# Kernel optimization log

Hardware: AMD Instinct MI355X
Metric: run time of the kernel (lower is better)

## Reference

```python
import jax, jax.numpy as jnp
import numpy as np

D = 512; NH = 8; NL = 6; DFF = 2048
TOK = 1024; APP = 3; V = TOK + APP; PAD = V - 1
B = 256; SENC = 16; LTGT = 62


def setup_inputs() -> dict:
    key = jax.random.key(0)
    ks = jax.random.split(key, 14)
    g = lambda k, shp, s=0.02: jax.random.normal(k, shp, jnp.float32) * s
    return dict(
        encoder_out=jax.random.normal(ks[0], (B, SENC, D), jnp.float32),
        point_out=jax.random.normal(ks[1], (B, D), jnp.float32),
        emb=g(ks[2], (V, D)),
        pos_embed=g(ks[3], (1, LTGT, D)),
        sa_inw=g(ks[4], (NL, 3 * D, D)), sa_inb=jnp.zeros((NL, 3 * D), jnp.float32),
        sa_outw=g(ks[5], (NL, D, D)), sa_outb=jnp.zeros((NL, D), jnp.float32),
        ca_inw=g(ks[6], (NL, 3 * D, D)), ca_inb=jnp.zeros((NL, 3 * D), jnp.float32),
        ca_outw=g(ks[7], (NL, D, D)), ca_outb=jnp.zeros((NL, D), jnp.float32),
        ln1_s=jnp.ones((NL, D), jnp.float32), ln1_b=jnp.zeros((NL, D), jnp.float32),
        ln2_s=jnp.ones((NL, D), jnp.float32), ln2_b=jnp.zeros((NL, D), jnp.float32),
        ln3_s=jnp.ones((NL, D), jnp.float32), ln3_b=jnp.zeros((NL, D), jnp.float32),
        ff1_w=g(ks[8], (NL, DFF, D)), ff1_b=jnp.zeros((NL, DFF), jnp.float32),
        ff2_w=g(ks[9], (NL, D, DFF)), ff2_b=jnp.zeros((NL, D), jnp.float32),
        out_w=g(ks[10], (V, D)), out_b=jnp.zeros((V,), jnp.float32),
        tgt=jax.random.randint(ks[11], (B, LTGT), 0, TOK),
    )


def _ln(x, s, b, eps=1e-5):
    m = x.mean(-1, keepdims=True)
    v = ((x - m) ** 2).mean(-1, keepdims=True)
    return (x - m) / jnp.sqrt(v + eps) * s + b


def _mha(q_in, kv_in, inw, inb, outw, outb, mask):
    # PyTorch MultiheadAttention with packed in_proj [3D, D]
    hd = D // NH
    wq, wk, wv = inw[:D], inw[D:2 * D], inw[2 * D:]
    bq, bk, bv = inb[:D], inb[D:2 * D], inb[2 * D:]
    Bq, Tq = q_in.shape[0], q_in.shape[1]
    Tk = kv_in.shape[1]
    q = (q_in @ wq.T + bq).reshape(Bq, Tq, NH, hd)
    k = (kv_in @ wk.T + bk).reshape(Bq, Tk, NH, hd)
    v = (kv_in @ wv.T + bv).reshape(Bq, Tk, NH, hd)
    s = jnp.einsum('bqhd,bkhd->bhqk', q, k) / np.float32(np.sqrt(hd))
    if mask is not None:
        s = s + mask
    a = jax.nn.softmax(s, axis=-1)
    o = jnp.einsum('bhqk,bkhd->bqhd', a, v).reshape(Bq, Tq, D)
    return o @ outw.T + outb


def reference(encoder_out, point_out, emb, pos_embed,
              sa_inw, sa_inb, sa_outw, sa_outb,
              ca_inw, ca_inb, ca_outw, ca_outb,
              ln1_s, ln1_b, ln2_s, ln2_b, ln3_s, ln3_b,
              ff1_w, ff1_b, ff2_w, ff2_b, out_w, out_b, tgt):
    # scheduled_sampling_ratio == 1.0 => the per-step loop always writes the
    # ground-truth token, so output_sequence == tgt[:, :-1] and the returned
    # tensor equals one full causal decoder pass over tgt[:, :-1].
    tokens = tgt[:, :-1]                      # [B, L], L = 61
    L = tokens.shape[1]
    neg = jnp.float32(-jnp.inf)
    causal = jnp.where(jnp.triu(jnp.ones((L, L), bool), 1), neg, 0.0)
    padm = jnp.where(tokens == PAD, neg, 0.0)[:, None, None, :]  # [B,1,1,L]
    mask = causal[None, None] + padm          # [B,1,L,L]
    mem = encoder_out[:, :1, :]               # memory length 1 (encoder_out[:, [0]])
    x = emb[tokens] + point_out[:, None, :] + pos_embed[0, :L]
    for i in range(NL):
        x = _ln(x + _mha(x, x, sa_inw[i], sa_inb[i], sa_outw[i], sa_outb[i], mask), ln1_s[i], ln1_b[i])
        x = _ln(x + _mha(x, mem, ca_inw[i], ca_inb[i], ca_outw[i], ca_outb[i], None), ln2_s[i], ln2_b[i])
        h = jax.nn.relu(x @ ff1_w[i].T + ff1_b[i]) @ ff2_w[i].T + ff2_b[i]
        x = _ln(x + h, ln3_s[i], ln3_b[i])
    return x @ out_w.T + out_b               # [B, L, V]
```

## Files before the change

kernel.cpp:

```cpp
#include <hip/hip_runtime.h>
#include <stdint.h>
#include <stddef.h>

typedef unsigned short u16;
typedef float f4 __attribute__((ext_vector_type(4)));
typedef float f32x4 __attribute__((ext_vector_type(4)));
typedef short bf16x8 __attribute__((ext_vector_type(8)));
typedef u16 u16x4 __attribute__((ext_vector_type(4)));
typedef int i4v __attribute__((ext_vector_type(4)));

#define PAD_TOK 1026
#define LQ 61
#define NBATCH 256
#define MTOT (NBATCH * LQ)

__device__ __forceinline__ u16 f2b(float f) {
  uint32_t x = __float_as_uint(f);
  x += 0x7fff + ((x >> 16) & 1);
  return (u16)(x >> 16);
}
__device__ __forceinline__ float b2f(u16 u) {
  return __uint_as_float(((uint32_t)u) << 16);
}
__device__ __forceinline__ u16x4 cvt4(f4 v) {
  return (u16x4){f2b(v[0]), f2b(v[1]), f2b(v[2]), f2b(v[3])};
}

#define GLDS(gptr, lptr) __builtin_amdgcn_global_load_lds( \
    (const __attribute__((address_space(1))) void*)(gptr), \
    (__attribute__((address_space(3))) void*)(lptr), 16, 0, 0)

__device__ __forceinline__ bf16x8 ldfrag(const u16* buf, int row, int ksl, int kg) {
  const int chunk = (ksl * 4 + kg) ^ (row & 7);
  return *(const bf16x8*)&buf[row * 64 + chunk * 8];
}

__global__ __launch_bounds__(512) void gemm_bt2(
    const u16* __restrict__ A, const u16* __restrict__ W,
    const float* __restrict__ bias,
    float* __restrict__ Cf, u16* __restrict__ Cb,
    int N, int K, int Nreal, int ldc, int relu)
{
  __shared__ u16 SH[384 * 64];
  u16* const As = SH;
  u16* const Bs = SH + 8192;

  const int gx = gridDim.x;
  const int nwg = gx * gridDim.y;
  const int orig = blockIdx.y * gx + blockIdx.x;
  const int q8 = nwg >> 3, r8 = nwg & 7;
  const int xcd = orig & 7, off = orig >> 3;
  const int nid = (xcd < r8 ? xcd * (q8 + 1) : r8 * (q8 + 1) + (xcd - r8) * q8) + off;
  const int bx = nid % gx, by = nid / gx;

  const int tid = threadIdx.x;
  const int wid = tid >> 6, lane = tid & 63;
  const int wm = wid >> 2, wn = wid & 3;
  const long m0 = (long)by * 128;
  const long n0 = (long)bx * 256;

  const int lr = lane >> 3;
  const int lc = lane & 7;
  const int scol = ((lc ^ lr) << 3);

  f32x4 acc[4][4];
#pragma unroll
  for (int i = 0; i < 4; ++i)
#pragma unroll
    for (int j = 0; j < 4; ++j) acc[i][j] = (f32x4){0.f, 0.f, 0.f, 0.f};

  const u16* Abase = A + m0 * K;
  const u16* Wbase = W + n0 * K;
  const int r = lane & 15, kg = lane >> 4;

  for (int kt = 0; kt < K; kt += 64) {
#pragma unroll
    for (int c = 0; c < 2; ++c) {
      const int row = wid * 16 + c * 8;
      GLDS(Abase + (long)(row + lr) * K + kt + scol, &As[row * 64]);
    }
#pragma unroll
    for (int c = 0; c < 4; ++c) {
      const int row = wid * 32 + c * 8;
      GLDS(Wbase + (long)(row + lr) * K + kt + scol, &Bs[row * 64]);
    }
    __syncthreads();

#pragma unroll
    for (int ks = 0; ks < 2; ++ks) {
      bf16x8 a[4], b[4];
#pragma unroll
      for (int mi = 0; mi < 4; ++mi)
        a[mi] = ldfrag(As, wm * 64 + mi * 16 + r, ks, kg);
#pragma unroll
      for (int ni = 0; ni < 4; ++ni)
        b[ni] = ldfrag(Bs, wn * 64 + ni * 16 + r, ks, kg);
#pragma unroll
      for (int mi = 0; mi < 4; ++mi)
#pragma unroll
        for (int ni = 0; ni < 4; ++ni)
          acc[mi][ni] = __builtin_amdgcn_mfma_f32_16x16x32_bf16(a[mi], b[ni], acc[mi][ni], 0, 0, 0);
    }
    __syncthreads();
  }

  const int cr4 = (lane >> 4) * 4;
  const int cc = lane & 15;

  if (Cb) {
#pragma unroll
    for (int half = 0; half < 2; ++half) {
      if (wm == half) {
#pragma unroll
        for (int ni = 0; ni < 4; ++ni) {
          const int coll = wn * 64 + ni * 16 + cc;
          const float bv = bias[(int)n0 + coll];
#pragma unroll
          for (int mi = 0; mi < 4; ++mi) {
#pragma unroll
            for (int j = 0; j < 4; ++j) {
              const int rowl = mi * 16 + cr4 + j;
              float v = acc[mi][ni][j] + bv;
              if (relu) v = fmaxf(v, 0.f);
              const int phys = (coll >> 3) ^ (rowl & 31);
              SH[rowl * 256 + phys * 8 + (coll & 7)] = f2b(v);
            }
          }
        }
      }
      __syncthreads();
#pragma unroll
      for (int i = 0; i < 4; ++i) {
        const int t = i * 512 + tid;
        const int row = t >> 5, ch = t & 31;
        const int n = (int)n0 + ch * 8;
        if (n < Nreal) {
          const int phys = ch ^ (row & 31);
          *(bf16x8*)&Cb[(m0 + half * 64 + row) * (long)N + n] =
              *(const bf16x8*)&SH[row * 256 + phys * 8];
        }
      }
      __syncthreads();
    }
  } else {
    float* SHf = (float*)SH;
#pragma unroll
    for (int q = 0; q < 4; ++q) {
      if (wm == (q >> 1)) {
        const int mib = (q & 1) * 2;
#pragma unroll
        for (int ni = 0; ni < 4; ++ni) {
          const int coll = wn * 64 + ni * 16 + cc;
          const float bv = bias[(int)n0 + coll];
#pragma unroll
          for (int mi2 = 0; mi2 < 2; ++mi2) {
#pragma unroll
            for (int j = 0; j < 4; ++j) {
              const int rowl = mi2 * 16 + cr4 + j;
              float v = acc[mib + mi2][ni][j] + bv;
              if (relu) v = fmaxf(v, 0.f);
              SHf[rowl * 260 + coll] = v;
            }
          }
        }
      }
      __syncthreads();
      {
        const int row = tid >> 4, c = tid & 15;
        const int nbase = (int)n0 + c * 16;
        const long gro = (m0 + q * 32 + row) * (long)ldc;
        if (nbase + 16 <= Nreal) {
#pragma unroll
          for (int e = 0; e < 16; ++e)
            Cf[gro + nbase + e] = SHf[row * 260 + c * 16 + e];
        } else if (nbase < Nreal) {
          for (int e = 0; e < Nreal - nbase; ++e)
            Cf[gro + nbase + e] = SHf[row * 260 + c * 16 + e];
        }
      }
      __syncthreads();
    }
  }
}

__global__ __launch_bounds__(512) void gemm_bt3(
    const u16* __restrict__ A, const u16* __restrict__ W,
    const float* __restrict__ bias, u16* __restrict__ Cb,
    int N, int K, int relu)
{
  __shared__ u16 SH[320 * 64];
  u16* const As = SH;
  u16* const Bs = SH + 4096;

  const int gx = gridDim.x;
  const int nwg = gx * gridDim.y;
  const int orig = blockIdx.y * gx + blockIdx.x;
  const int q8 = nwg >> 3, r8 = nwg & 7;
  const int xcd = orig & 7, off = orig >> 3;
  const int nid = (xcd < r8 ? xcd * (q8 + 1) : r8 * (q8 + 1) + (xcd - r8) * q8) + off;
  const int bx = nid % gx, by = nid / gx;

  const int tid = threadIdx.x;
  const int wid = tid >> 6, lane = tid & 63;
  const int wm = wid >> 2, wn = wid & 3;
  const long m0 = (long)by * 64;
  const long n0 = (long)bx * 256;

  const int lr = lane >> 3;
  const int lc = lane & 7;
  const int scol = ((lc ^ lr) << 3);

  f32x4 acc[2][4];
#pragma unroll
  for (int i = 0; i < 2; ++i)
#pragma unroll
    for (int j = 0; j < 4; ++j) acc[i][j] = (f32x4){0.f, 0.f, 0.f, 0.f};

  const u16* Abase = A + m0 * K;
  const u16* Wbase = W + n0 * K;
  const int r = lane & 15, kg = lane >> 4;

  for (int kt = 0; kt < K; kt += 64) {
    {
      const int arow = wid * 8;
      GLDS(Abase + (long)(arow + lr) * K + kt + scol, &As[arow * 64]);
#pragma unroll
      for (int c = 0; c < 4; ++c) {
        const int row = wid * 32 + c * 8;
        GLDS(Wbase + (long)(row + lr) * K + kt + scol, &Bs[row * 64]);
      }
    }
    __syncthreads();

#pragma unroll
    for (int ks = 0; ks < 2; ++ks) {
      bf16x8 a0 = ldfrag(As, wm * 32 + r, ks, kg);
      bf16x8 a1 = ldfrag(As, wm * 32 + 16 + r, ks, kg);
#pragma unroll
      for (int ni = 0; ni < 4; ++ni) {
        bf16x8 b = ldfrag(Bs, wn * 64 + ni * 16 + r, ks, kg);
        acc[0][ni] = __builtin_amdgcn_mfma_f32_16x16x32_bf16(a0, b, acc[0][ni], 0, 0, 0);
        acc[1][ni] = __builtin_amdgcn_mfma_f32_16x16x32_bf16(a1, b, acc[1][ni], 0, 0, 0);
      }
    }
    __syncthreads();
  }

  const int cr4 = (lane >> 4) * 4;
  const int cc = lane & 15;

#pragma unroll
  for (int ni = 0; ni < 4; ++ni) {
    const int coll = wn * 64 + ni * 16 + cc;
    const float bv = bias[(int)n0 + coll];
#pragma unroll
    for (int mi = 0; mi < 2; ++mi) {
#pragma unroll
      for (int j = 0; j < 4; ++j) {
        const int rowl = wm * 32 + mi * 16 + cr4 + j;
        float v = acc[mi][ni][j] + bv;
        if (relu) v = fmaxf(v, 0.f);
        const int phys = (coll >> 3) ^ (rowl & 31);
        SH[rowl * 256 + phys * 8 + (coll & 7)] = f2b(v);
      }
    }
  }
  __syncthreads();
#pragma unroll
  for (int i = 0; i < 4; ++i) {
    const int t = i * 512 + tid;
    const int row = t >> 5, ch = t & 31;
    const int n = (int)n0 + ch * 8;
    const int phys = ch ^ (row & 31);
    *(bf16x8*)&Cb[(m0 + row) * (long)N + n] =
        *(const bf16x8*)&SH[row * 256 + phys * 8];
  }
}

template<int BM>
__global__ __launch_bounds__(256) void gemm_bt(
    const u16* __restrict__ A, const u16* __restrict__ W,
    const float* __restrict__ bias,
    float* __restrict__ Cf, u16* __restrict__ Cb,
    int M, int N, int K, int Nreal, int ldc, int relu,
    long aZ, long wZ, long bZ, long cZ)
{
  constexpr int MI = BM / 32;
  const int z = blockIdx.z;
  A += z * aZ; W += z * wZ; bias += z * bZ;
  if (Cf) Cf += z * cZ;
  if (Cb) Cb += z * cZ;

  __shared__ u16 As[BM * 64];
  __shared__ u16 Bs[128 * 64];

  const int gx = gridDim.x;
  const int nwg = gx * gridDim.y;
  const int orig = blockIdx.y * gx + blockIdx.x;
  const int q8 = nwg >> 3, r8 = nwg & 7;
  const int xcd = orig & 7, off = orig >> 3;
  const int nid = (xcd < r8 ? xcd * (q8 + 1) : r8 * (q8 + 1) + (xcd - r8) * q8) + off;
  const int bx = nid % gx, by = nid / gx;

  const int tid = threadIdx.x;
  const int wid = tid >> 6, lane = tid & 63;
  const int wr = wid >> 1, wc = wid & 1;
  const long m0 = (long)by * BM;
  const long n0 = (long)bx * 128;

  const int lr = lane >> 3;
  const int lc = lane & 7;
  const int scol = ((lc ^ lr) << 3);

  f32x4 acc[MI][4];
#pragma unroll
  for (int i = 0; i < MI; ++i)
#pragma unroll
    for (int j = 0; j < 4; ++j) acc[i][j] = (f32x4){0.f, 0.f, 0.f, 0.f};

  const u16* Abase = A + m0 * K;
  const u16* Wbase = W + n0 * K;
  const int r = lane & 15, kg = lane >> 4;

  for (int kt = 0; kt < K; kt += 64) {
#pragma unroll
    for (int c = 0; c < BM / 32; ++c) {
      const int row = wid * (BM / 4) + c * 8;
      GLDS(Abase + (long)(row + lr) * K + kt + scol, &As[row * 64]);
    }
#pragma unroll
    for (int c = 0; c < 4; ++c) {
      const int row = wid * 32 + c * 8;
      GLDS(Wbase + (long)(row + lr) * K + kt + scol, &Bs[row * 64]);
    }
    __syncthreads();

#pragma unroll
    for (int ks = 0; ks < 2; ++ks) {
      bf16x8 a[MI], b[4];
#pragma unroll
      for (int mi = 0; mi < MI; ++mi)
        a[mi] = ldfrag(As, wr * (BM / 2) + mi * 16 + r, ks, kg);
#pragma unroll
      for (int ni = 0; ni < 4; ++ni)
        b[ni] = ldfrag(Bs, wc * 64 + ni * 16 + r, ks, kg);
#pragma unroll
      for (int mi = 0; mi < MI; ++mi)
#pragma unroll
        for (int ni = 0; ni < 4; ++ni)
          acc[mi][ni] = __builtin_amdgcn_mfma_f32_16x16x32_bf16(a[mi], b[ni], acc[mi][ni], 0, 0, 0);
    }
    __syncthreads();
  }

  const int cr4 = (lane >> 4) * 4;
  const int cc = lane & 15;

  if (Cb) {
#pragma unroll
    for (int ni = 0; ni < 4; ++ni) {
      const int coll = wc * 64 + ni * 16 + cc;
      const float bv = bias[(int)n0 + coll];
#pragma unroll
      for (int mi = 0; mi < MI; ++mi) {
#pragma unroll
        for (int j = 0; j < 4; ++j) {
          const int rowl = wr * (BM / 2) + mi * 16 + cr4 + j;
          float v = acc[mi][ni][j] + bv;
          if (relu) v = fmaxf(v, 0.f);
          const int sw = (rowl & 7) << 3;
          u16* half = (coll & 64) ? Bs : As;
          half[rowl * 64 + ((coll & 63) ^ sw)] = f2b(v);
        }
      }
    }
    __syncthreads();
    constexpr int PT = BM / 16;
#pragma unroll
    for (int i = 0; i < PT; ++i) {
      const int t = i * 256 + tid;
      const int row = t >> 4, ch = t & 15;
      const int n = (int)n0 + ch * 8;
      if (n < Nreal) {
        const int phys = (ch & 7) ^ (row & 7);
        const u16* half = (ch < 8) ? As : Bs;
        bf16x8 vv = *(const bf16x8*)&half[row * 64 + phys * 8];
        *(bf16x8*)&Cb[(m0 + row) * (long)N + n] = vv;
      }
    }
  } else {
#pragma unroll
    for (int ni = 0; ni < 4; ++ni) {
      const int n = (int)n0 + wc * 64 + ni * 16 + cc;
      if (n >= Nreal) continue;
      const float bv = bias[n];
#pragma unroll
      for (int mi = 0; mi < MI; ++mi) {
#pragma unroll
        for (int j = 0; j < 4; ++j) {
          const long m = m0 + wr * (BM / 2) + mi * 16 + cr4 + j;
          float v = acc[mi][ni][j] + bv;
          if (relu) v = fmaxf(v, 0.f);
          Cf[m * ldc + n] = v;
        }
      }
    }
  }
}

__global__ __launch_bounds__(512) void gemmln_k(
    const u16* __restrict__ A, const u16* __restrict__ W,
    const float* __restrict__ bias,
    const u16* __restrict__ cavb,
    const float* __restrict__ s1w, const float* __restrict__ b1w,
    const float* __restrict__ s2w, const float* __restrict__ b2w,
    u16* __restrict__ XB, int K)
{
  __shared__ u16 LDSBUF[2][36864];
  __shared__ float LSTAT[64][8];
  __shared__ u16 LCAV[1536];
  u16* const EP = &LDSBUF[0][0];

  const int nwg = gridDim.x;
  const int orig = blockIdx.x;
  const int q8 = nwg >> 3, r8 = nwg & 7;
  const int xcd = orig & 7, off = orig >> 3;
  const int by = (xcd < r8 ? xcd * (q8 + 1) : r8 * (q8 + 1) + (xcd - r8) * q8) + off;

  const int tid = threadIdx.x;
  const int wid = tid >> 6, lane = tid & 63;
  const int wm = wid >> 2, wn = wid & 3;
  const long m0 = (long)by * 64;

  const int lr = lane >> 3, lc = lane & 7;
  const int scol = ((lc ^ lr) << 3);
  const int r = lane & 15, kg = lane >> 4;

  f32x4 acc[2][8];
#pragma unroll
  for (int i = 0; i < 2; ++i)
#pragma unroll
    for (int j = 0; j < 8; ++j) acc[i][j] = (f32x4){0.f, 0.f, 0.f, 0.f};

  const u16* Abase = A + m0 * K;

#define STAGE(buf, kt) do {                                              \
    const int arow_ = wid * 8;                                           \
    GLDS(Abase + (long)(arow_ + lr) * K + (kt) + scol,                   \
         &(buf)[32768 + arow_ * 64]);                                    \
    _Pragma("unroll")                                                    \
    for (int c_ = 0; c_ < 8; ++c_) {                                     \
      const int row_ = wid * 64 + c_ * 8;                                \
      GLDS(W + (long)(row_ + lr) * K + (kt) + scol, &(buf)[row_ * 64]);  \
    }                                                                    \
  } while (0)

  const int nt = K >> 6;
  STAGE(LDSBUF[0], 0);
  asm volatile("s_waitcnt vmcnt(0)" ::: "memory");
  __builtin_amdgcn_sched_barrier(0);
  __builtin_amdgcn_s_barrier();

  for (int t = 0; t < nt; ++t) {
    u16* const bufc = &LDSBUF[t & 1][0];
    if (t + 1 < nt) STAGE(LDSBUF[(t + 1) & 1], (t + 1) << 6);
#pragma unroll
    for (int ks = 0; ks < 2; ++ks) {
      bf16x8 a0 = ldfrag(bufc + 32768, wm * 32 + r, ks, kg);
      bf16x8 a1 = ldfrag(bufc + 32768, wm * 32 + 16 + r, ks, kg);
      __builtin_amdgcn_s_setprio(1);
#pragma unroll
      for (int ni = 0; ni < 8; ++ni) {
        bf16x8 b = ldfrag(bufc, wn * 128 + ni * 16 + r, ks, kg);
        acc[0][ni] = __builtin_amdgcn_mfma_f32_16x16x32_bf16(a0, b, acc[0][ni], 0, 0, 0);
        acc[1][ni] = __builtin_amdgcn_mfma_f32_16x16x32_bf16(a1, b, acc[1][ni], 0, 0, 0);
      }
      __builtin_amdgcn_s_setprio(0);
    }
    asm volatile("s_waitcnt vmcnt(0)" ::: "memory");
    __builtin_amdgcn_sched_barrier(0);
    __builtin_amdgcn_s_barrier();
  }
#undef STAGE

  const int b0 = (int)(m0 / LQ);
  const int bsplit1 = (b0 + 1) * LQ;
  const int bsplit2 = (b0 + 2) * LQ;

#pragma unroll
  for (int i = 0; i < 8; ++i) {
    const int t = i * 512 + tid;
    const int row = t >> 6, ch = t & 63;
    *(bf16x8*)&EP[row * 516 + ch * 8] =
        *(const bf16x8*)&XB[(m0 + row) * 512 + ch * 8];
  }
  for (int t = tid; t < 1536; t += 512) {
    const int bb = t >> 9, c = t & 511;
    int bi = b0 + bb;
    if (bi > NBATCH - 1) bi = NBATCH - 1;
    LCAV[bb * 512 + c] = cavb[(long)bi * 512 + c];
  }
  __syncthreads();

  float bcol[8];
#pragma unroll
  for (int ni = 0; ni < 8; ++ni) bcol[ni] = bias[wn * 128 + ni * 16 + r];
#pragma unroll
  for (int mi = 0; mi < 2; ++mi)
#pragma unroll
    for (int ni = 0; ni < 8; ++ni) {
      const int col = wn * 128 + ni * 16 + r;
#pragma unroll
      for (int j = 0; j < 4; ++j) {
        const int row = wm * 32 + mi * 16 + kg * 4 + j;
        acc[mi][ni][j] += bcol[ni] + b2f(EP[row * 516 + col]);
      }
    }

#pragma unroll
  for (int mi = 0; mi < 2; ++mi)
#pragma unroll
    for (int j = 0; j < 4; ++j) {
      float s1 = 0.f, s2 = 0.f;
#pragma unroll
      for (int ni = 0; ni < 8; ++ni) {
        const float v = acc[mi][ni][j];
        s1 += v; s2 += v * v;
      }
#pragma unroll
      for (int o = 1; o < 16; o <<= 1) {
        s1 += __shfl_xor(s1, o);
        s2 += __shfl_xor(s2, o);
      }
      if (r == 0) {
        const int row = wm * 32 + mi * 16 + kg * 4 + j;
        LSTAT[row][wn] = s1;
        LSTAT[row][4 + wn] = s2;
      }
    }
  __syncthreads();

  float sc[8], bc[8];
#pragma unroll
  for (int ni = 0; ni < 8; ++ni) {
    const int col = wn * 128 + ni * 16 + r;
    sc[ni] = s1w[col]; bc[ni] = b1w[col];
  }
#pragma unroll
  for (int mi = 0; mi < 2; ++mi)
#pragma unroll
    for (int j = 0; j < 4; ++j) {
      const int row = wm * 32 + mi * 16 + kg * 4 + j;
      const float S1 = LSTAT[row][0] + LSTAT[row][1] + LSTAT[row][2] + LSTAT[row][3];
      const float S2 = LSTAT[row][4] + LSTAT[row][5] + LSTAT[row][6] + LSTAT[row][7];
      const float mean = S1 * (1.f / 512.f);
      const float var = S2 * (1.f / 512.f) - mean * mean;
      const float rstd = rsqrtf(var + 1e-5f);
#pragma unroll
      for (int ni = 0; ni < 8; ++ni)
        acc[mi][ni][j] = (acc[mi][ni][j] - mean) * rstd * sc[ni] + bc[ni];
    }

#pragma unroll
  for (int mi = 0; mi < 2; ++mi)
#pragma unroll
    for (int j = 0; j < 4; ++j) {
      const int row = wm * 32 + mi * 16 + kg * 4 + j;
      const int gr = (int)m0 + row;
      const int sel = (gr >= bsplit2) ? 2 : ((gr >= bsplit1) ? 1 : 0);
#pragma unroll
      for (int ni = 0; ni < 8; ++ni) {
        const int col = wn * 128 + ni * 16 + r;
        acc[mi][ni][j] += b2f(LCAV[sel * 512 + col]);
      }
    }
  __syncthreads();
#pragma unroll
  for (int mi = 0; mi < 2; ++mi)
#pragma unroll
    for (int j = 0; j < 4; ++j) {
      float s1 = 0.f, s2 = 0.f;
#pragma unroll
      for (int ni = 0; ni < 8; ++ni) {
        const float v = acc[mi][ni][j];
        s1 += v; s2 += v * v;
      }
#pragma unroll
      for (int o = 1; o < 16; o <<= 1) {
        s1 += __shfl_xor(s1, o);
        s2 += __shfl_xor(s2, o);
      }
      if (r == 0) {
        const int row = wm * 32 + mi * 16 + kg * 4 + j;
        LSTAT[row][wn] = s1;
        LSTAT[row][4 + wn] = s2;
      }
    }
  __syncthreads();
#pragma unroll
  for (int ni = 0; ni < 8; ++ni) {
    const int col = wn * 128 + ni * 16 + r;
    sc[ni] = s2w[col]; bc[ni] = b2w[col];
  }
#pragma unroll
  for (int mi = 0; mi < 2; ++mi)
#pragma unroll
    for (int j = 0; j < 4; ++j) {
      const int row = wm * 32 + mi * 16 + kg * 4 + j;
      const float S1 = LSTAT[row][0] + LSTAT[row][1] + LSTAT[row][2] + LSTAT[row][3];
      const float S2 = LSTAT[row][4] + LSTAT[row][5] + LSTAT[row][6] + LSTAT[row][7];
      const float mean = S1 * (1.f / 512.f);
      const float var = S2 * (1.f / 512.f) - mean * mean;
      const float rstd = rsqrtf(var + 1e-5f);
#pragma unroll
      for (int ni = 0; ni < 8; ++ni)
        acc[mi][ni][j] = (acc[mi][ni][j] - mean) * rstd * sc[ni] + bc[ni];
    }

#pragma unroll
  for (int mi = 0; mi < 2; ++mi)
#pragma unroll
    for (int ni = 0; ni < 8; ++ni) {
      const int col = wn * 128 + ni * 16 + r;
#pragma unroll
      for (int j = 0; j < 4; ++j) {
        const int row = wm * 32 + mi * 16 + kg * 4 + j;
        EP[row * 516 + col] = f2b(acc[mi][ni][j]);
      }
    }
  __syncthreads();
#pragma unroll
  for (int i = 0; i < 8; ++i) {
    const int t = i * 512 + tid;
    const int row = t >> 6, ch = t & 63;
    *(bf16x8*)&XB[(m0 + row) * 512 + ch * 8] =
        *(const bf16x8*)&EP[row * 516 + ch * 8];
  }
}

__global__ __launch_bounds__(256) void attn_k(const u16* __restrict__ qkv,
                                              const int* __restrict__ tgt,
                                              u16* __restrict__ outp)
{
  __shared__ u16 Qs[64 * 72];
  __shared__ u16 Ks[64 * 72];
  __shared__ u16 Vt[64 * 72];
  __shared__ float S[64 * 65];
  __shared__ int stok[64];

  const int bid = blockIdx.x;
  const int b = bid >> 3, h = bid & 7;
  const int tid = threadIdx.x;
  const int tr = tid >> 2, seg = tid & 3;

  if (tid < 64) stok[tid] = (tid < 61) ? tgt[b * 62 + tid] : -1;

  const long rowbase = ((long)(b * LQ + tr)) * 1536 + h * 64;
  if (tr < LQ) {
    const i4v* qsrc = (const i4v*)(qkv + rowbase + seg * 16);
    i4v q0 = qsrc[0], q1 = qsrc[1];
    *(i4v*)&Qs[tr * 72 + seg * 16] = q0;
    *(i4v*)&Qs[tr * 72 + seg * 16 + 8] = q1;
    const i4v* ksrc = (const i4v*)(qkv + rowbase + 512 + seg * 16);
    i4v k0 = ksrc[0], k1 = ksrc[1];
    *(i4v*)&Ks[tr * 72 + seg * 16] = k0;
    *(i4v*)&Ks[tr * 72 + seg * 16 + 8] = k1;
    const u16* vsrc = qkv + rowbase + 1024 + seg * 16;
#pragma unroll
    for (int i = 0; i < 16; ++i) Vt[(seg * 16 + i) * 72 + tr] = vsrc[i];
  } else {
    i4v zz = {0, 0, 0, 0};
    *(i4v*)&Qs[tr * 72 + seg * 16] = zz;
    *(i4v*)&Qs[tr * 72 + seg * 16 + 8] = zz;
    *(i4v*)&Ks[tr * 72 + seg * 16] = zz;
    *(i4v*)&Ks[tr * 72 + seg * 16 + 8] = zz;
#pragma unroll
    for (int i = 0; i < 16; ++i) Vt[(seg * 16 + i) * 72 + tr] = 0;
  }
  __syncthreads();

  const int lane = tid & 63, w = tid >> 6;
  const int r = lane & 15, kg = lane >> 4;

  {
    f32x4 s[4];
#pragma unroll
    for (int ni = 0; ni < 4; ++ni) s[ni] = (f32x4){0.f, 0.f, 0.f, 0.f};
    bf16x8 a0 = *(const bf16x8*)&Qs[(w * 16 + r) * 72 + kg * 8];
    bf16x8 a1 = *(const bf16x8*)&Qs[(w * 16 + r) * 72 + 32 + kg * 8];
#pragma unroll
    for (int ni = 0; ni < 4; ++ni) {
      bf16x8 b0 = *(const bf16x8*)&Ks[(ni * 16 + r) * 72 + kg * 8];
      bf16x8 b1 = *(const bf16x8*)&Ks[(ni * 16 + r) * 72 + 32 + kg * 8];
      s[ni] = __builtin_amdgcn_mfma_f32_16x16x32_bf16(a0, b0, s[ni], 0, 0, 0);
      s[ni] = __builtin_amdgcn_mfma_f32_16x16x32_bf16(a1, b1, s[ni], 0, 0, 0);
    }
#pragma unroll
    for (int ni = 0; ni < 4; ++ni)
#pragma unroll
      for (int j = 0; j < 4; ++j)
        S[(w * 16 + kg * 4 + j) * 65 + ni * 16 + r] = s[ni][j];
  }
  __syncthreads();

  {
    const int row = tid >> 2, g = tid & 3;
    float vals[16];
    float mx = -3e38f;
#pragma unroll
    for (int i = 0; i < 16; ++i) {
      const int k = g * 16 + i;
      float v = S[row * 65 + k] * 0.125f;
      const bool ok = (k <= row) && (k < LQ) && (stok[k] != PAD_TOK);
      v = ok ? v : -1e30f;
      vals[i] = v;
      mx = fmaxf(mx, v);
    }
    mx = fmaxf(mx, __shfl_xor(mx, 1));
    mx = fmaxf(mx, __shfl_xor(mx, 2));
    float sum = 0.f;
#pragma unroll
    for (int i = 0; i < 16; ++i) { float e = __expf(vals[i] - mx); vals[i] = e; sum += e; }
    sum += __shfl_xor(sum, 1);
    sum += __shfl_xor(sum, 2);
    const float inv = 1.f / sum;
#pragma unroll
    for (int i = 0; i < 16; ++i) Qs[row * 72 + g * 16 + i] = f2b(vals[i] * inv);
  }
  __syncthreads();

  {
    f32x4 o[4];
#pragma unroll
    for (int ni = 0; ni < 4; ++ni) o[ni] = (f32x4){0.f, 0.f, 0.f, 0.f};
    bf16x8 a0 = *(const bf16x8*)&Qs[(w * 16 + r) * 72 + kg * 8];
    bf16x8 a1 = *(const bf16x8*)&Qs[(w * 16 + r) * 72 + 32 + kg * 8];
#pragma unroll
    for (int ni = 0; ni < 4; ++ni) {
      bf16x8 b0 = *(const bf16x8*)&Vt[(ni * 16 + r) * 72 + kg * 8];
      bf16x8 b1 = *(const bf16x8*)&Vt[(ni * 16 + r) * 72 + 32 + kg * 8];
      o[ni] = __builtin_amdgcn_mfma_f32_16x16x32_bf16(a0, b0, o[ni], 0, 0, 0);
      o[ni] = __builtin_amdgcn_mfma_f32_16x16x32_bf16(a1, b1, o[ni], 0, 0, 0);
    }
#pragma unroll
    for (int ni = 0; ni < 4; ++ni)
#pragma unroll
      for (int j = 0; j < 4; ++j) {
        const int qrow = w * 16 + kg * 4 + j;
        const int col = ni * 16 + r;
        Ks[qrow * 64 + (col ^ ((qrow & 7) << 3))] = f2b(o[ni][j]);
      }
  }
  __syncthreads();

  {
    const int row = tid >> 2, sub = tid & 3;
    if (row < LQ) {
      const long obase = ((long)(b * LQ + row)) * 512 + h * 64;
#pragma unroll
      for (int i = 0; i < 2; ++i) {
        const int ch = i * 4 + sub;
        const int phys = ch ^ (row & 7);
        bf16x8 vv = *(const bf16x8*)&Ks[row * 64 + phys * 8];
        *(bf16x8*)&outp[obase + ch * 8] = vv;
      }
    }
  }
}

__device__ __forceinline__ void ln_row(f4& v0, f4& v1,
                                       const float* __restrict__ sw,
                                       const float* __restrict__ bw, int d0) {
  float s1 = v0[0] + v0[1] + v0[2] + v0[3] + v1[0] + v1[1] + v1[2] + v1[3];
  float s2 = v0[0]*v0[0] + v0[1]*v0[1] + v0[2]*v0[2] + v0[3]*v0[3]
           + v1[0]*v1[0] + v1[1]*v1[1] + v1[2]*v1[2] + v1[3]*v1[3];
#pragma unroll
  for (int off = 1; off < 64; off <<= 1) {
    s1 += __shfl_xor(s1, off);
    s2 += __shfl_xor(s2, off);
  }
  const float mean = s1 * (1.f / 512.f);
  const float var = s2 * (1.f / 512.f) - mean * mean;
  const float rstd = rsqrtf(var + 1e-5f);
  const f4* sp = (const f4*)(sw + d0);
  const f4* bp = (const f4*)(bw + d0);
  f4 ss0 = sp[0], ss1 = sp[1], bb0 = bp[0], bb1 = bp[1];
#pragma unroll
  for (int i = 0; i < 4; ++i) {
    v0[i] = (v0[i] - mean) * rstd * ss0[i] + bb0[i];
    v1[i] = (v1[i] - mean) * rstd * ss1[i] + bb1[i];
  }
}

__global__ __launch_bounds__(256) void lnf3_k(const u16* __restrict__ p,
                                              const u16* __restrict__ xr,
                                              const float* __restrict__ s1,
                                              const float* __restrict__ b1,
                                              u16* __restrict__ out)
{
  const int m = blockIdx.x * 4 + (threadIdx.x >> 6);
  const int lane = threadIdx.x & 63;
  const int d0 = lane * 8;
  bf16x8 pv = *(const bf16x8*)(p + (long)m * 512 + d0);
  bf16x8 xv = *(const bf16x8*)(xr + (long)m * 512 + d0);
  f4 v0, v1;
#pragma unroll
  for (int i = 0; i < 4; ++i) {
    v0[i] = b2f((u16)pv[i]) + b2f((u16)xv[i]);
    v1[i] = b2f((u16)pv[4 + i]) + b2f((u16)xv[4 + i]);
  }
  ln_row(v0, v1, s1, b1, d0);
  u16x4* ob = (u16x4*)(out + (long)m * 512 + d0);
  ob[0] = cvt4(v0);
  ob[1] = cvt4(v1);
}

__global__ __launch_bounds__(256) void embed_k(const float* __restrict__ emb,
                                               const float* __restrict__ pout,
                                               const float* __restrict__ pos,
                                               const int* __restrict__ tgt,
                                               u16* __restrict__ XB)
{
  const int m = blockIdx.x * 4 + (threadIdx.x >> 6);
  const int lane = threadIdx.x & 63;
  const int b = m / LQ, t = m % LQ;
  const int tok = tgt[b * 62 + t];
  const int d0 = lane * 8;
  const f4* e = (const f4*)(emb + (long)tok * 512 + d0);
  const f4* p = (const f4*)(pout + (long)b * 512 + d0);
  const f4* q = (const f4*)(pos + (long)t * 512 + d0);
  f4 v0 = e[0] + p[0] + q[0];
  f4 v1 = e[1] + p[1] + q[1];
  u16x4* xb = (u16x4*)(XB + (long)m * 512 + d0);
  xb[0] = cvt4(v0);
  xb[1] = cvt4(v1);
}

__global__ void cvtall_k(const float* __restrict__ sa_inw, const float* __restrict__ sa_outw,
                         const float* __restrict__ ca_outw, const float* __restrict__ ff1_w,
                         const float* __restrict__ ff2_w, const float* __restrict__ ca_inw,
                         const float* __restrict__ out_w, const float* __restrict__ out_b,
                         const float* __restrict__ enc,
                         u16* __restrict__ WSA, u16* __restrict__ WSO,
                         u16* __restrict__ WCO, u16* __restrict__ WF1,
                         u16* __restrict__ WF2, u16* __restrict__ WCAV,
                         u16* __restrict__ WOUT, float* __restrict__ BOUT,
                         u16* __restrict__ MEMB)
{
  const int C0 = 320;
  const int C1 = C0 + 32768;
  const int C2 = C1 + 163840;
  const int C3 = C2 + 393216;
  const int C4 = C3 + 1179648;
  const int C5 = C4 + 393216;
  const int C6 = C5 + 393216;
  const int C7 = C6 + 1572864;
  const int C8 = C7 + 1572864;
  for (int i = blockIdx.x * 256 + threadIdx.x; i < C8; i += gridDim.x * 256) {
    if (i < C0) {
      const int base = i * 4;
#pragma unroll
      for (int e = 0; e < 4; ++e)
        BOUT[base + e] = (base + e < 1027) ? out_b[base + e] : 0.f;
    } else if (i < C1) {
      const int k = i - C0;
      const int b = (k * 4) >> 9, d = (k * 4) & 511;
      f4 v = ((const f4*)enc)[(b * 8192 + d) >> 2];
      ((u16x4*)MEMB)[k] = cvt4(v);
    } else if (i < C2) {
      const int k = i - C1;
      const int row = (k * 4) >> 9;
      u16x4 o = {0, 0, 0, 0};
      if (row < 1027) { f4 v = ((const f4*)out_w)[k]; o = cvt4(v); }
      ((u16x4*)WOUT)[k] = o;
    } else if (i < C3) {
      const int k = i - C2;
      const int l = k >> 16, rem = k & 65535;
      f4 v = ((const f4*)ca_inw)[l * 196608 + 131072 + rem];
      ((u16x4*)WCAV)[k] = cvt4(v);
    } else {
      const float* s; u16* d; int k;
      if (i < C4)      { s = sa_inw;  d = WSA; k = i - C3; }
      else if (i < C5) { s = sa_outw; d = WSO; k = i - C4; }
      else if (i < C6) { s = ca_outw; d = WCO; k = i - C5; }
      else if (i < C7) { s = ff1_w;   d = WF1; k = i - C6; }
      else             { s = ff2_w;   d = WF2; k = i - C7; }
      f4 v = ((const f4*)s)[k];
      ((u16x4*)d)[k] = cvt4(v);
    }
  }
}

static constexpr size_t XB_OFF    = 0;
static constexpr size_t P_OFF     = 15990784;
static constexpr size_t BIG_OFF   = 31981568;
static constexpr size_t ATT_OFF   = 95944704;
static constexpr size_t WSA_OFF   = 111935488;
static constexpr size_t WSO_OFF   = 121372672;
static constexpr size_t WCAV_OFF  = 124518400;
static constexpr size_t WCO_OFF   = 127664128;
static constexpr size_t WF1_OFF   = 130809856;
static constexpr size_t WF2_OFF   = 143392768;
static constexpr size_t WOUT_OFF  = 155975680;
static constexpr size_t BOUT_OFF  = 157286400;
static constexpr size_t MEMB_OFF  = 157291520;
static constexpr size_t CATMP_OFF = 157553664;
static constexpr size_t CAVB_OFF  = 159126528;

extern "C" void kernel_launch(void* const* d_in, const int* in_sizes, int n_in,
                              void* d_out, int out_size, void* d_ws, size_t ws_size,
                              hipStream_t stream) {
  (void)in_sizes; (void)n_in; (void)out_size; (void)ws_size;
  const float* encoder_out = (const float*)d_in[0];
  const float* point_out   = (const float*)d_in[1];
  const float* emb         = (const float*)d_in[2];
  const float* pos         = (const float*)d_in[3];
  const float* sa_inw      = (const float*)d_in[4];
  const float* sa_inb      = (const float*)d_in[5];
  const float* sa_outw     = (const float*)d_in[6];
  const float* sa_outb     = (const float*)d_in[7];
  const float* ca_inw      = (const float*)d_in[8];
  const float* ca_inb      = (const float*)d_in[9];
  const float* ca_outw     = (const float*)d_in[10];
  const float* ca_outb     = (const float*)d_in[11];
  const float* ln1_s       = (const float*)d_in[12];
  const float* ln1_b       = (const float*)d_in[13];
  const float* ln2_s       = (const float*)d_in[14];
  const float* ln2_b       = (const float*)d_in[15];
  const float* ln3_s       = (const float*)d_in[16];
  const float* ln3_b       = (const float*)d_in[17];
  const float* ff1_w       = (const float*)d_in[18];
  const float* ff1_b       = (const float*)d_in[19];
  const float* ff2_w       = (const float*)d_in[20];
  const float* ff2_b       = (const float*)d_in[21];
  const float* out_w       = (const float*)d_in[22];
  const float* out_b       = (const float*)d_in[23];
  const int*   tgt         = (const int*)d_in[24];

  char* ws = (char*)d_ws;
  u16*   XB    = (u16*)(ws + XB_OFF);
  u16*   P     = (u16*)(ws + P_OFF);
  u16*   BIG   = (u16*)(ws + BIG_OFF);
  u16*   ATT   = (u16*)(ws + ATT_OFF);
  u16*   WSA   = (u16*)(ws + WSA_OFF);
  u16*   WSO   = (u16*)(ws + WSO_OFF);
  u16*   WCAV  = (u16*)(ws + WCAV_OFF);
  u16*   WCO   = (u16*)(ws + WCO_OFF);
  u16*   WF1   = (u16*)(ws + WF1_OFF);
  u16*   WF2   = (u16*)(ws + WF2_OFF);
  u16*   WOUT  = (u16*)(ws + WOUT_OFF);
  float* BOUT  = (float*)(ws + BOUT_OFF);
  u16*   MEMB  = (u16*)(ws + MEMB_OFF);
  u16*   CATMP = (u16*)(ws + CATMP_OFF);
  u16*   CAVB  = (u16*)(ws + CAVB_OFF);

  cvtall_k<<<dim3(2048), dim3(256), 0, stream>>>(
      sa_inw, sa_outw, ca_outw, ff1_w, ff2_w, ca_inw, out_w, out_b, encoder_out,
      WSA, WSO, WCO, WF1, WF2, WCAV, WOUT, BOUT, MEMB);

  embed_k<<<dim3(MTOT / 4), dim3(256), 0, stream>>>(emb, point_out, pos, tgt, XB);

  gemm_bt<64><<<dim3(4, 4, 6), dim3(256), 0, stream>>>(
      MEMB, WCAV, ca_inb + 1024, nullptr, CATMP,
      256, 512, 512, 512, 512, 0,
      0L, 262144L, 1536L, 131072L);
  gemm_bt<64><<<dim3(4, 4, 6), dim3(256), 0, stream>>>(
      CATMP, WCO, ca_outb, nullptr, CAVB,
      256, 512, 512, 512, 512, 0,
      131072L, 262144L, 512L, 131072L);

  for (int l = 0; l < 6; ++l) {
    gemm_bt2<<<dim3(6, 122), dim3(512), 0, stream>>>(
        XB, WSA + (long)l * 786432, sa_inb + l * 1536, nullptr, BIG,
        1536, 512, 1536, 1536, 0);
    attn_k<<<dim3(2048), dim3(256), 0, stream>>>(BIG, tgt, ATT);
    gemmln_k<<<dim3(244), dim3(512), 0, stream>>>(
        ATT, WSO + (long)l * 262144, sa_outb + l * 512,
        CAVB + (long)l * 131072,
        ln1_s + l * 512, ln1_b + l * 512, ln2_s + l * 512, ln2_b + l * 512,
        XB, 512);
    gemm_bt2<<<dim3(8, 122), dim3(512), 0, stream>>>(
        XB, WF1 + (long)l * 1048576, ff1_b + l * 2048, nullptr, BIG,
        2048, 512, 2048, 2048, 1);
    gemm_bt3<<<dim3(2, 244), dim3(512), 0, stream>>>(
        BIG, WF2 + (long)l * 1048576, ff2_b + l * 512, P,
        512, 2048, 0);
    lnf3_k<<<dim3(MTOT / 4), dim3(256), 0, stream>>>(
        P, XB, ln3_s + l * 512, ln3_b + l * 512, XB);
  }

  gemm_bt2<<<dim3(5, 122), dim3(512), 0, stream>>>(
      XB, WOUT, BOUT, (float*)d_out, nullptr,
      1280, 512, 1027, 1027, 0);
}
```

Baseline: 1.110 ms.

## Use 64-row double-buffered GEMM for QKV, FF1 and output projections

Replaces the 128x256-tile GEMM used for the QKV, FF1 and vocabulary projections with a new 64x256-tile kernel that double-buffers LDS. It issues the next tile's global-to-LDS loads before computing the current one and waits with a partial vmcnt. The smaller tile doubles the workgroup count for better CU fill. The gemmln kernel's prefetch loop is also changed to wait with a partial vmcnt before the barrier rather than draining all loads at the end of each iteration. This trades lower per-block data reuse and more redundant weight loads for more parallelism and overlap of memory with MFMA work.

```diff
diff --git a/kernel.cpp b/kernel.cpp
--- a/kernel.cpp
+++ b/kernel.cpp
@@ -35,15 +35,15 @@
   return *(const bf16x8*)&buf[row * 64 + chunk * 8];
 }
 
-__global__ __launch_bounds__(512) void gemm_bt2(
+__global__ __launch_bounds__(512) void gemm_bt3(
     const u16* __restrict__ A, const u16* __restrict__ W,
     const float* __restrict__ bias,
     float* __restrict__ Cf, u16* __restrict__ Cb,
     int N, int K, int Nreal, int ldc, int relu)
 {
-  __shared__ u16 SH[384 * 64];
+  __shared__ u16 SH[320 * 64];
   u16* const As = SH;
-  u16* const Bs = SH + 8192;
+  u16* const Bs = SH + 4096;
 
   const int gx = gridDim.x;
   const int nwg = gx * gridDim.y;
@@ -56,16 +56,16 @@
   const int tid = threadIdx.x;
   const int wid = tid >> 6, lane = tid & 63;
   const int wm = wid >> 2, wn = wid & 3;
-  const long m0 = (long)by * 128;
+  const long m0 = (long)by * 64;
   const long n0 = (long)bx * 256;
 
   const int lr = lane >> 3;
   const int lc = lane & 7;
   const int scol = ((lc ^ lr) << 3);
 
-  f32x4 acc[4][4];
-#pragma unroll
-  for (int i = 0; i < 4; ++i)
+  f32x4 acc[2][4];
+#pragma unroll
+  for (int i = 0; i < 2; ++i)
 #pragma unroll
     for (int j = 0; j < 4; ++j) acc[i][j] = (f32x4){0.f, 0.f, 0.f, 0.f};
 
@@ -74,32 +74,29 @@
   const int r = lane & 15, kg = lane >> 4;
 
   for (int kt = 0; kt < K; kt += 64) {
-#pragma unroll
-    for (int c = 0; c < 2; ++c) {
-      const int row = wid * 16 + c * 8;
-      GLDS(Abase + (long)(row + lr) * K + kt + scol, &As[row * 64]);
-    }
-#pragma unroll
-    for (int c = 0; c < 4; ++c) {
-      const int row = wid * 32 + c * 8;
-      GLDS(Wbase + (long)(row + lr) * K + kt + scol, &Bs[row * 64]);
+    {
+      const int arow = wid * 8;
+      GLDS(Abase + (long)(arow + lr) * K + kt + scol, &As[arow * 64]);
+#pragma unroll
+      for (int c = 0; c < 4; ++c) {
+        const int row = wid * 32 + c * 8;
+        GLDS(Wbase + (long)(row + lr) * K + kt + scol, &Bs[row * 64]);
+      }
     }
     __syncthreads();
 
 #pragma unroll
     for (int ks = 0; ks < 2; ++ks) {
-      bf16x8 a[4], b[4];
-#pragma unroll
-      for (int mi = 0; mi < 4; ++mi)
-        a[mi] = ldfrag(As, wm * 64 + mi * 16 + r, ks, kg);
-#pragma unroll
-      for (int ni = 0; ni < 4; ++ni)
-        b[ni] = ldfrag(Bs, wn * 64 + ni * 16 + r, ks, kg);
-#pragma unroll
-      for (int mi = 0; mi < 4; ++mi)
-#pragma unroll
-        for (int ni = 0; ni < 4; ++ni)
-          acc[mi][ni] = __builtin_amdgcn_mfma_f32_16x16x32_bf16(a[mi], b[ni], acc[mi][ni], 0, 0, 0);
+      bf16x8 a0 = ldfrag(As, wm * 32 + r, ks, kg);
+      bf16x8 a1 = ldfrag(As, wm * 32 + 16 + r, ks, kg);
+      __builtin_amdgcn_s_setprio(1);
+#pragma unroll
+      for (int ni = 0; ni < 4; ++ni) {
+        bf16x8 b = ldfrag(Bs, wn * 64 + ni * 16 + r, ks, kg);
+        acc[0][ni] = __builtin_amdgcn_mfma_f32_16x16x32_bf16(a0, b, acc[0][ni], 0, 0, 0);
+        acc[1][ni] = __builtin_amdgcn_mfma_f32_16x16x32_bf16(a1, b, acc[1][ni], 0, 0, 0);
+      }
+      __builtin_amdgcn_s_setprio(0);
     }
     __syncthreads();
   }
@@ -109,55 +106,46 @@
 
   if (Cb) {
 #pragma unroll
-    for (int half = 0; half < 2; ++half) {
-      if (wm == half) {
+    for (int ni = 0; ni < 4; ++ni) {
+      const int coll = wn * 64 + ni * 16 + cc;
+      const float bv = bias[(int)n0 + coll];
+#pragma unroll
+      for (int mi = 0; mi < 2; ++mi) {
+#pragma unroll
+        for (int j = 0; j < 4; ++j) {
+          const int rowl = wm * 32 + mi * 16 + cr4 + j;
+          float v = acc[mi][ni][j] + bv;
+          if (relu) v = fmaxf(v, 0.f);
+          const int phys = (coll >> 3) ^ (rowl & 31);
+          SH[rowl * 256 + phys * 8 + (coll & 7)] = f2b(v);
+        }
+      }
+    }
+    __syncthreads();
+#pragma unroll
+    for (int i = 0; i < 4; ++i) {
+      const int t = i * 512 + tid;
+      const int row = t >> 5, ch = t & 31;
+      const int n = (int)n0 + ch * 8;
+      const int phys = ch ^ (row & 31);
+      *(bf16x8*)&Cb[(m0 + row) * (long)N + n] =
+          *(const bf16x8*)&SH[row * 256 + phys * 8];
+    }
+  } else {
+    float* SHf = (float*)SH;
+#pragma unroll
+    for (int p = 0; p < 2; ++p) {
+      if (wm == p) {
 #pragma unroll
         for (int ni = 0; ni < 4; ++ni) {
           const int coll = wn * 64 + ni * 16 + cc;
           const float bv = bias[(int)n0 + coll];
 #pragma unroll
-          for (int mi = 0; mi < 4; ++mi) {
+          for (int mi = 0; mi < 2; ++mi) {
 #pragma unroll
             for (int j = 0; j < 4; ++j) {
               const int rowl = mi * 16 + cr4 + j;
               float v = acc[mi][ni][j] + bv;
-              if (relu) v = fmaxf(v, 0.f);
-              const int phys = (coll >> 3) ^ (rowl & 31);
-              SH[rowl * 256 + phys * 8 + (coll & 7)] = f2b(v);
-            }
-          }
-        }
-      }
-      __syncthreads();
-#pragma unroll
-      for (int i = 0; i < 4; ++i) {
-        const int t = i * 512 + tid;
-        const int row = t >> 5, ch = t & 31;
-        const int n = (int)n0 + ch * 8;
-        if (n < Nreal) {
-          const int phys = ch ^ (row & 31);
-          *(bf16x8*)&Cb[(m0 + half * 64 + row) * (long)N + n] =
-              *(const bf16x8*)&SH[row * 256 + phys * 8];
-        }
-      }
-      __syncthreads();
-    }
-  } else {
-    float* SHf = (float*)SH;
-#pragma unroll
-    for (int q = 0; q < 4; ++q) {
-      if (wm == (q >> 1)) {
-        const int mib = (q & 1) * 2;
-#pragma unroll
-        for (int ni = 0; ni < 4; ++ni) {
-          const int coll = wn * 64 + ni * 16 + cc;
-          const float bv = bias[(int)n0 + coll];
-#pragma unroll
-          for (int mi2 = 0; mi2 < 2; ++mi2) {
-#pragma unroll
-            for (int j = 0; j < 4; ++j) {
-              const int rowl = mi2 * 16 + cr4 + j;
-              float v = acc[mib + mi2][ni][j] + bv;
               if (relu) v = fmaxf(v, 0.f);
               SHf[rowl * 260 + coll] = v;
             }
@@ -168,7 +156,7 @@
       {
         const int row = tid >> 4, c = tid & 15;
         const int nbase = (int)n0 + c * 16;
-        const long gro = (m0 + q * 32 + row) * (long)ldc;
+        const long gro = (m0 + p * 32 + row) * (long)ldc;
         if (nbase + 16 <= Nreal) {
 #pragma unroll
           for (int e = 0; e < 16; ++e)
@@ -183,14 +171,13 @@
   }
 }
 
-__global__ __launch_bounds__(512) void gemm_bt3(
+__global__ __launch_bounds__(512) void gemm_bt3p(
     const u16* __restrict__ A, const u16* __restrict__ W,
-    const float* __restrict__ bias, u16* __restrict__ Cb,
-    int N, int K, int relu)
+    const float* __restrict__ bias,
+    float* __restrict__ Cf, u16* __restrict__ Cb,
+    int N, int K, int Nreal, int ldc, int relu)
 {
-  __shared__ u16 SH[320 * 64];
-  u16* const As = SH;
-  u16* const Bs = SH + 4096;
+  __shared__ u16 SH[2][20480];
 
   const int gx = gridDim.x;
   const int nwg = gx * gridDim.y;
@@ -220,60 +207,118 @@
   const u16* Wbase = W + n0 * K;
   const int r = lane & 15, kg = lane >> 4;
 
-  for (int kt = 0; kt < K; kt += 64) {
-    {
-      const int arow = wid * 8;
-      GLDS(Abase + (long)(arow + lr) * K + kt + scol, &As[arow * 64]);
-#pragma unroll
-      for (int c = 0; c < 4; ++c) {
-        const int row = wid * 32 + c * 8;
-        GLDS(Wbase + (long)(row + lr) * K + kt + scol, &Bs[row * 64]);
-      }
-    }
-    __syncthreads();
+#define STG(buf, kt) do {                                                   \
+    const int arow_ = wid * 8;                                              \
+    GLDS(Abase + (long)(arow_ + lr) * K + (kt) + scol, &(buf)[arow_ * 64]); \
+    _Pragma("unroll")                                                       \
+    for (int c_ = 0; c_ < 4; ++c_) {                                        \
+      const int row_ = wid * 32 + c_ * 8;                                   \
+      GLDS(Wbase + (long)(row_ + lr) * K + (kt) + scol,                     \
+           &(buf)[4096 + row_ * 64]);                                       \
+    }                                                                       \
+  } while (0)
+
+  const int nt = K >> 6;
+  STG(SH[0], 0);
+
+  for (int t = 0; t < nt; ++t) {
+    u16* const cur = SH[t & 1];
+    if (t + 1 < nt) {
+      STG(SH[(t + 1) & 1], (t + 1) << 6);
+      asm volatile("s_waitcnt vmcnt(5)" ::: "memory");
+    } else {
+      asm volatile("s_waitcnt vmcnt(0)" ::: "memory");
+    }
+    __builtin_amdgcn_sched_barrier(0);
+    __builtin_amdgcn_s_barrier();
+    __builtin_amdgcn_sched_barrier(0);
 
 #pragma unroll
     for (int ks = 0; ks < 2; ++ks) {
-      bf16x8 a0 = ldfrag(As, wm * 32 + r, ks, kg);
-      bf16x8 a1 = ldfrag(As, wm * 32 + 16 + r, ks, kg);
+      bf16x8 a0 = ldfrag(cur, wm * 32 + r, ks, kg);
+      bf16x8 a1 = ldfrag(cur, wm * 32 + 16 + r, ks, kg);
+      __builtin_amdgcn_s_setprio(1);
 #pragma unroll
       for (int ni = 0; ni < 4; ++ni) {
-        bf16x8 b = ldfrag(Bs, wn * 64 + ni * 16 + r, ks, kg);
+        bf16x8 b = ldfrag(cur + 4096, wn * 64 + ni * 16 + r, ks, kg);
         acc[0][ni] = __builtin_amdgcn_mfma_f32_16x16x32_bf16(a0, b, acc[0][ni], 0, 0, 0);
         acc[1][ni] = __builtin_amdgcn_mfma_f32_16x16x32_bf16(a1, b, acc[1][ni], 0, 0, 0);
       }
-    }
-    __syncthreads();
-  }
+      __builtin_amdgcn_s_setprio(0);
+    }
+    __builtin_amdgcn_sched_barrier(0);
+    __builtin_amdgcn_s_barrier();
+  }
+#undef STG
 
   const int cr4 = (lane >> 4) * 4;
   const int cc = lane & 15;
-
-#pragma unroll
-  for (int ni = 0; ni < 4; ++ni) {
-    const int coll = wn * 64 + ni * 16 + cc;
-    const float bv = bias[(int)n0 + coll];
-#pragma unroll
-    for (int mi = 0; mi < 2; ++mi) {
-#pragma unroll
-      for (int j = 0; j < 4; ++j) {
-        const int rowl = wm * 32 + mi * 16 + cr4 + j;
-        float v = acc[mi][ni][j] + bv;
-        if (relu) v = fmaxf(v, 0.f);
-        const int phys = (coll >> 3) ^ (rowl & 31);
-        SH[rowl * 256 + phys * 8 + (coll & 7)] = f2b(v);
-      }
-    }
-  }
-  __syncthreads();
-#pragma unroll
-  for (int i = 0; i < 4; ++i) {
-    const int t = i * 512 + tid;
-    const int row = t >> 5, ch = t & 31;
-    const int n = (int)n0 + ch * 8;
-    const int phys = ch ^ (row & 31);
-    *(bf16x8*)&Cb[(m0 + row) * (long)N + n] =
-        *(const bf16x8*)&SH[row * 256 + phys * 8];
+  u16* const EP = &SH[0][0];
+
+  if (Cb) {
+#pragma unroll
+    for (int ni = 0; ni < 4; ++ni) {
+      const int coll = wn * 64 + ni * 16 + cc;
+      const float bv = bias[(int)n0 + coll];
+#pragma unroll
+      for (int mi = 0; mi < 2; ++mi) {
+#pragma unroll
+        for (int j = 0; j < 4; ++j) {
+          const int rowl = wm * 32 + mi * 16 + cr4 + j;
+          float v = acc[mi][ni][j] + bv;
+          if (relu) v = fmaxf(v, 0.f);
+          const int phys = (coll >> 3) ^ (rowl & 31);
+          EP[rowl * 256 + phys * 8 + (coll & 7)] = f2b(v);
+        }
+      }
+    }
+    __syncthreads();
+#pragma unroll
+    for (int i = 0; i < 4; ++i) {
+      const int t = i * 512 + tid;
+      const int row = t >> 5, ch = t & 31;
+      const int n = (int)n0 + ch * 8;
+      const int phys = ch ^ (row & 31);
+      *(bf16x8*)&Cb[(m0 + row) * (long)N + n] =
+          *(const bf16x8*)&EP[row * 256 + phys * 8];
+    }
+  } else {
+    float* SHf = (float*)EP;
+#pragma unroll
+    for (int p = 0; p < 2; ++p) {
+      if (wm == p) {
+#pragma unroll
+        for (int ni = 0; ni < 4; ++ni) {
+          const int coll = wn * 64 + ni * 16 + cc;
+          const float bv = bias[(int)n0 + coll];
+#pragma unroll
+          for (int mi = 0; mi < 2; ++mi) {
+#pragma unroll
+            for (int j = 0; j < 4; ++j) {
+              const int rowl = mi * 16 + cr4 + j;
+              float v = acc[mi][ni][j] + bv;
+              if (relu) v = fmaxf(v, 0.f);
+              SHf[rowl * 260 + coll] = v;
+            }
+          }
+        }
+      }
+      __syncthreads();
+      {
+        const int row = tid >> 4, c = tid & 15;
+        const int nbase = (int)n0 + c * 16;
+        const long gro = (m0 + p * 32 + row) * (long)ldc;
+        if (nbase + 16 <= Nreal) {
+#pragma unroll
+          for (int e = 0; e < 16; ++e)
+            Cf[gro + nbase + e] = SHf[row * 260 + c * 16 + e];
+        } else if (nbase < Nreal) {
+          for (int e = 0; e < Nreal - nbase; ++e)
+            Cf[gro + nbase + e] = SHf[row * 260 + c * 16 + e];
+        }
+      }
+      __syncthreads();
+    }
   }
 }
 
@@ -457,13 +502,18 @@
 
   const int nt = K >> 6;
   STAGE(LDSBUF[0], 0);
-  asm volatile("s_waitcnt vmcnt(0)" ::: "memory");
-  __builtin_amdgcn_sched_barrier(0);
-  __builtin_amdgcn_s_barrier();
 
   for (int t = 0; t < nt; ++t) {
     u16* const bufc = &LDSBUF[t & 1][0];
-    if (t + 1 < nt) STAGE(LDSBUF[(t + 1) & 1], (t + 1) << 6);
+    if (t + 1 < nt) {
+      STAGE(LDSBUF[(t + 1) & 1], (t + 1) << 6);
+      asm volatile("s_waitcnt vmcnt(9)" ::: "memory");
+    } else {
+      asm volatile("s_waitcnt vmcnt(0)" ::: "memory");
+    }
+    __builtin_amdgcn_sched_barrier(0);
+    __builtin_amdgcn_s_barrier();
+    __builtin_amdgcn_sched_barrier(0);
 #pragma unroll
     for (int ks = 0; ks < 2; ++ks) {
       bf16x8 a0 = ldfrag(bufc + 32768, wm * 32 + r, ks, kg);
@@ -477,7 +527,6 @@
       }
       __builtin_amdgcn_s_setprio(0);
     }
-    asm volatile("s_waitcnt vmcnt(0)" ::: "memory");
     __builtin_amdgcn_sched_barrier(0);
     __builtin_amdgcn_s_barrier();
   }
@@ -957,7 +1006,6 @@
   cvtall_k<<<dim3(2048), dim3(256), 0, stream>>>(
       sa_inw, sa_outw, ca_outw, ff1_w, ff2_w, ca_inw, out_w, out_b, encoder_out,
       WSA, WSO, WCO, WF1, WF2, WCAV, WOUT, BOUT, MEMB);
-
   embed_k<<<dim3(MTOT / 4), dim3(256), 0, stream>>>(emb, point_out, pos, tgt, XB);
 
   gemm_bt<64><<<dim3(4, 4, 6), dim3(256), 0, stream>>>(
@@ -970,7 +1018,7 @@
       131072L, 262144L, 512L, 131072L);
 
   for (int l = 0; l < 6; ++l) {
-    gemm_bt2<<<dim3(6, 122), dim3(512), 0, stream>>>(
+    gemm_bt3p<<<dim3(6, 244), dim3(512), 0, stream>>>(
         XB, WSA + (long)l * 786432, sa_inb + l * 1536, nullptr, BIG,
         1536, 512, 1536, 1536, 0);
     attn_k<<<dim3(2048), dim3(256), 0, stream>>>(BIG, tgt, ATT);
@@ -979,17 +1027,17 @@
         CAVB + (long)l * 131072,
         ln1_s + l * 512, ln1_b + l * 512, ln2_s + l * 512, ln2_b + l * 512,
         XB, 512);
-    gemm_bt2<<<dim3(8, 122), dim3(512), 0, stream>>>(
+    gemm_bt3p<<<dim3(8, 244), dim3(512), 0, stream>>>(
         XB, WF1 + (long)l * 1048576, ff1_b + l * 2048, nullptr, BIG,
         2048, 512, 2048, 2048, 1);
     gemm_bt3<<<dim3(2, 244), dim3(512), 0, stream>>>(
-        BIG, WF2 + (long)l * 1048576, ff2_b + l * 512, P,
-        512, 2048, 0);
+        BIG, WF2 + (long)l * 1048576, ff2_b + l * 512, nullptr, P,
+        512, 2048, 512, 512, 0);
     lnf3_k<<<dim3(MTOT / 4), dim3(256), 0, stream>>>(
         P, XB, ln3_s + l * 512, ln3_b + l * 512, XB);
   }
 
-  gemm_bt2<<<dim3(5, 122), dim3(512), 0, stream>>>(
+  gemm_bt3p<<<dim3(5, 244), dim3(512), 0, stream>>>(
       XB, WOUT, BOUT, (float*)d_out, nullptr,
       1280, 512, 1027, 1027, 0);
 }
```

Result: slower. 1.146 ms (+3.3%).
